# Performance work log

Measured on AMD Instinct MI355X. Metric: run time of the kernel, lower is better.

## Reference

```python
import jax, jax.numpy as jnp
import numpy as np
from jax import lax

CI, CO, K = 4096, 256, 4
COKK = CO * K * K  # 4096


def setup_inputs() -> dict:
    key = jax.random.key(0)
    k1, k2 = jax.random.split(key)
    U = jax.random.normal(k1, (CI, CI), dtype=jnp.float32) * 0.05
    V = jax.random.normal(k2, (COKK, COKK), dtype=jnp.float32) * 0.05
    return {"U": U, "V": V}


def _q(V):
    """Product of d Householder reflections H(v_0) ... H(v_{d-1}).
    Faithful to: M = I; for i in range(d): M = M @ (I - 2 v_i v_i^T),
    but applied as a rank-1 update M -= 2 (M v) v^T via lax.scan.
    """
    d = V.shape[0]
    # torch.norm(V.T, 2, dim=1) == column norms of V
    norms = jnp.linalg.norm(V, axis=0)
    Vn = V / norms[None, :]

    def step(M, v):
        Mv = M @ v  # [d]
        return M - 2.0 * jnp.outer(Mv, v), None

    M0 = jnp.eye(d, dtype=V.dtype)
    M, _ = lax.scan(step, M0, Vn.T)  # iterate over columns in order
    return M


def reference(U, V):
    Qu = _q(U)  # [ci, ci]
    Qv = _q(V)  # [cokk, cokk]
    if CI < COKK:
        W = Qu @ Qv[:CI, :]
    else:
        W = Qu[:, :COKK] @ Qv
    W = W.reshape(1, CI, CO, K, K)
    # original forward runs entirely under torch.no_grad()
    return lax.stop_gradient(W)
```

## Files before the change

kernel.cpp:

```cpp
#include <hip/hip_runtime.h>
#include <hip/hip_bf16.h>


#define N4K 4096
#define ELN ((long)N4K * (long)N4K)

typedef __bf16 bf16x8 __attribute__((ext_vector_type(8)));
typedef float f32x4 __attribute__((ext_vector_type(4)));

__device__ __forceinline__ unsigned short f2bf(float x) {
    unsigned int u = __builtin_bit_cast(unsigned int, x);
    u += 0x7FFFu + ((u >> 16) & 1u);
    return (unsigned short)(u >> 16);
}
__device__ __forceinline__ float bf2f(unsigned short h) {
    unsigned int u = ((unsigned int)h) << 16;
    return __builtin_bit_cast(float, u);
}
__device__ __forceinline__ void split_store(float v, unsigned short* H, unsigned short* L, long idx) {
    unsigned short h = f2bf(v);
    H[idx] = h;
    L[idx] = f2bf(v - bf2f(h));
}

__global__ __launch_bounds__(256) void colnorm2_k(const float* __restrict__ A, float* __restrict__ out) {
    int col = blockIdx.x * 256 + threadIdx.x;
    long r0 = (long)blockIdx.y * 128;
    float s = 0.f;
    for (int r = 0; r < 128; ++r) {
        float v = A[(r0 + r) * N4K + col];
        s += v * v;
    }
    atomicAdd(&out[col], s);
}

__global__ __launch_bounds__(256) void rsqrt_k(float* x) {
    int i = blockIdx.x * 256 + threadIdx.x;
    x[i] = 1.0f / sqrtf(x[i]);
}

__global__ __launch_bounds__(256) void normalize_split_k(const float* __restrict__ A, const float* __restrict__ rn,
                                                         unsigned short* __restrict__ H, unsigned short* __restrict__ L) {
    long i = ((long)blockIdx.x * 256 + threadIdx.x) * 4;
    float4 v = *(const float4*)(A + i);
    float4 rv = *(const float4*)(rn + (int)(i & (N4K - 1)));
    float a0 = v.x * rv.x, a1 = v.y * rv.y, a2 = v.z * rv.z, a3 = v.w * rv.w;
    ushort4 h, lo;
    h.x = f2bf(a0); lo.x = f2bf(a0 - bf2f(h.x));
    h.y = f2bf(a1); lo.y = f2bf(a1 - bf2f(h.y));
    h.z = f2bf(a2); lo.z = f2bf(a2 - bf2f(h.z));
    h.w = f2bf(a3); lo.w = f2bf(a3 - bf2f(h.w));
    *(ushort4*)(H + i) = h;
    *(ushort4*)(L + i) = lo;
}

__global__ __launch_bounds__(256) void transpose_split_k(const float* __restrict__ A, const float* __restrict__ rn,
                                                         unsigned short* __restrict__ H, unsigned short* __restrict__ L) {
    __shared__ float tile[64][65];
    int bj = blockIdx.x, bi = blockIdx.y;
    int t = threadIdx.x;
    int c = t & 63, r0 = t >> 6;
    for (int q = 0; q < 16; ++q) {
        int r = q * 4 + r0;
        tile[r][c] = A[(long)(bi * 64 + r) * N4K + bj * 64 + c];
    }
    __syncthreads();
    for (int q = 0; q < 16; ++q) {
        int orow = q * 4 + r0;
        int j = bj * 64 + orow;
        float v = tile[c][orow] * rn[j];
        long idx = (long)j * N4K + bi * 64 + c;
        unsigned short h = f2bf(v);
        H[idx] = h;
        L[idx] = f2bf(v - bf2f(h));
    }
}

__global__ __launch_bounds__(64) void tri_inv_base64_k(const unsigned short* __restrict__ Sh, const unsigned short* __restrict__ Sl,
                                                       unsigned short* __restrict__ Th, unsigned short* __restrict__ Tl,
                                                       unsigned short* __restrict__ Tth, unsigned short* __restrict__ Ttl) {
    __shared__ float R[64][65];
    __shared__ float X[64][65];
    int b0 = blockIdx.x * 64;
    int t = threadIdx.x;
    for (int r = 0; r < 64; ++r) {
        long idx = (long)(b0 + r) * N4K + b0 + t;
        float v = bf2f(Sh[idx]) + bf2f(Sl[idx]);
        R[r][t] = (t > r) ? v : 0.f;
    }
    __syncthreads();
    X[t][t] = 2.f;
    for (int i = t - 1; i >= 0; --i) {
        float s = 0.f;
        for (int k = i + 1; k <= t; ++k) s += R[i][k] * X[t][k];
        X[t][i] = -2.f * s;
    }
    __syncthreads();
    for (int r = 0; r < 64; ++r) {
        long idx = (long)(b0 + r) * N4K + b0 + t;
        float v = (t >= r) ? X[t][r] : 0.f;
        split_store(v, Th, Tl, idx);
        float vt = (r >= t) ? X[r][t] : 0.f;
        split_store(vt, Tth, Ttl, idx);
    }
}

__global__ __launch_bounds__(256) void combine64_k(const unsigned short* __restrict__ Sh, const unsigned short* __restrict__ Sl,
                                                   unsigned short* __restrict__ Th, unsigned short* __restrict__ Tl,
                                                   unsigned short* __restrict__ Tth, unsigned short* __restrict__ Ttl) {
    __shared__ float T11[64][65], T22[64][65], P[64][65];
    int p = blockIdx.x;
    int base = 128 * p;
    int t = threadIdx.x;
    for (int q = 0; q < 16; ++q) {
        int e = q * 256 + t;
        int r = e >> 6, c = e & 63;
        long i1 = (long)(base + r) * N4K + base + c;
        T11[r][c] = bf2f(Th[i1]) + bf2f(Tl[i1]);
        long i2 = (long)(base + 64 + r) * N4K + base + 64 + c;
        T22[r][c] = bf2f(Th[i2]) + bf2f(Tl[i2]);
    }
    __syncthreads();
    int j = t & 63, i0 = t >> 6;
    for (int i = i0; i < 64; i += 4) {
        float s = 0.f;
        for (int k = 0; k < 64; ++k) {
            long is = (long)(base + i) * N4K + base + 64 + k;
            float s12 = bf2f(Sh[is]) + bf2f(Sl[is]);
            s += s12 * T22[k][j];
        }
        P[i][j] = s;
    }
    __syncthreads();
    for (int i = i0; i < 64; i += 4) {
        float s = 0.f;
        for (int k = 0; k < 64; ++k) s += T11[i][k] * P[k][j];
        float v = -s;
        long it = (long)(base + i) * N4K + base + 64 + j;
        split_store(v, Th, Tl, it);
        long itt = (long)(base + 64 + j) * N4K + base + i;
        split_store(v, Tth, Ttl, itt);
    }
}

__global__ __launch_bounds__(256) void gemm_split_bt(
    const unsigned short* __restrict__ Ah, const unsigned short* __restrict__ Al, long lda, long sA,
    const unsigned short* __restrict__ Bh, const unsigned short* __restrict__ Bl, long ldb, long sB,
    float* __restrict__ Cf, unsigned short* __restrict__ Ch, unsigned short* __restrict__ Cl, long ldc, long sC,
    int K, float alpha, int addI) {
    __shared__ unsigned short sAh[128 * 32], sAl[128 * 32], sBh[128 * 32], sBl[128 * 32];
    int tid = threadIdx.x;
    int bx = blockIdx.x, by = blockIdx.y, bz = blockIdx.z;
    const unsigned short* pAh = Ah + (long)bz * sA + (long)by * 128 * lda;
    const unsigned short* pAl = Al + (long)bz * sA + (long)by * 128 * lda;
    const unsigned short* pBh = Bh + (long)bz * sB + (long)bx * 128 * ldb;
    const unsigned short* pBl = Bl + (long)bz * sB + (long)bx * 128 * ldb;
    int ilda = (int)lda, ildb = (int)ldb;

    int ch0 = tid, ch1 = tid + 256;
    int r0 = ch0 >> 2, c0 = ch0 & 3;
    int r1 = ch1 >> 2, c1 = ch1 & 3;
    int gA0 = r0 * ilda + c0 * 8, gA1 = r1 * ilda + c1 * 8;
    int gB0 = r0 * ildb + c0 * 8, gB1 = r1 * ildb + c1 * 8;
    int l0 = r0 * 32 + ((c0 ^ ((r0 >> 1) & 3)) << 3);
    int l1 = r1 * 32 + ((c1 ^ ((r1 >> 1) & 3)) << 3);

    int w = tid >> 6, l = tid & 63;
    int wm = w >> 1, wn = w & 1;
    int aoff[4], boff[4];
#pragma unroll
    for (int m = 0; m < 4; ++m) {
        int rowa = wm * 64 + m * 16 + (l & 15);
        aoff[m] = rowa * 32 + (((l >> 4) ^ ((rowa >> 1) & 3)) << 3);
        int rowb = wn * 64 + m * 16 + (l & 15);
        boff[m] = rowb * 32 + (((l >> 4) ^ ((rowb >> 1) & 3)) << 3);
    }

    f32x4 acc[4][4];
#pragma unroll
    for (int m = 0; m < 4; ++m)
#pragma unroll
        for (int n = 0; n < 4; ++n) acc[m][n] = (f32x4){0.f, 0.f, 0.f, 0.f};

    uint4 ra0 = *(const uint4*)(pAh + gA0), ra1 = *(const uint4*)(pAh + gA1);
    uint4 rb0 = *(const uint4*)(pAl + gA0), rb1 = *(const uint4*)(pAl + gA1);
    uint4 rc0 = *(const uint4*)(pBh + gB0), rc1 = *(const uint4*)(pBh + gB1);
    uint4 rd0 = *(const uint4*)(pBl + gB0), rd1 = *(const uint4*)(pBl + gB1);

    int nk = K >> 5;
#pragma unroll 1
    for (int kt = 0; kt < nk; ++kt) {
        __syncthreads();
        *(uint4*)&sAh[l0] = ra0; *(uint4*)&sAh[l1] = ra1;
        *(uint4*)&sAl[l0] = rb0; *(uint4*)&sAl[l1] = rb1;
        *(uint4*)&sBh[l0] = rc0; *(uint4*)&sBh[l1] = rc1;
        *(uint4*)&sBl[l0] = rd0; *(uint4*)&sBl[l1] = rd1;
        __syncthreads();
        if (kt + 1 < nk) {
            pAh += 32; pAl += 32; pBh += 32; pBl += 32;
            ra0 = *(const uint4*)(pAh + gA0); ra1 = *(const uint4*)(pAh + gA1);
            rb0 = *(const uint4*)(pAl + gA0); rb1 = *(const uint4*)(pAl + gA1);
            rc0 = *(const uint4*)(pBh + gB0); rc1 = *(const uint4*)(pBh + gB1);
            rd0 = *(const uint4*)(pBl + gB0); rd1 = *(const uint4*)(pBl + gB1);
        }
        bf16x8 fah[4], fal[4], fbh[4], fbl[4];
#pragma unroll
        for (int m = 0; m < 4; ++m) {
            fah[m] = *(const bf16x8*)&sAh[aoff[m]];
            fal[m] = *(const bf16x8*)&sAl[aoff[m]];
            fbh[m] = *(const bf16x8*)&sBh[boff[m]];
            fbl[m] = *(const bf16x8*)&sBl[boff[m]];
        }
#pragma unroll
        for (int m = 0; m < 4; ++m)
#pragma unroll
            for (int n = 0; n < 4; ++n) {
                acc[m][n] = __builtin_amdgcn_mfma_f32_16x16x32_bf16(fah[m], fbh[n], acc[m][n], 0, 0, 0);
                acc[m][n] = __builtin_amdgcn_mfma_f32_16x16x32_bf16(fah[m], fbl[n], acc[m][n], 0, 0, 0);
                acc[m][n] = __builtin_amdgcn_mfma_f32_16x16x32_bf16(fal[m], fbh[n], acc[m][n], 0, 0, 0);
            }
    }

    float* CfZ = Cf ? (Cf + (long)bz * sC) : nullptr;
    unsigned short* ChZ = Ch ? (Ch + (long)bz * sC) : nullptr;
    unsigned short* ClZ = Cl ? (Cl + (long)bz * sC) : nullptr;
    int r16 = (l >> 4) * 4, c16 = l & 15;
#pragma unroll
    for (int m = 0; m < 4; ++m)
#pragma unroll
        for (int n = 0; n < 4; ++n)
#pragma unroll
            for (int r = 0; r < 4; ++r) {
                int row = by * 128 + wm * 64 + m * 16 + r16 + r;
                int col = bx * 128 + wn * 64 + n * 16 + c16;
                float v = acc[m][n][r] * alpha;
                if (addI && row == col) v += 1.0f;
                long idx = (long)row * ldc + col;
                if (CfZ) CfZ[idx] = v;
                if (ChZ) {
                    unsigned short h = f2bf(v);
                    ChZ[idx] = h;
                    ClZ[idx] = f2bf(v - bf2f(h));
                }
            }
}

struct Bufs {
    unsigned short *Ah, *Al, *Th, *Tl, *Quh, *Qul, *Gh, *Gl;
    unsigned short *Sh, *Sl;
    float* rnorm;
};

static inline void launch_gemm(const unsigned short* Ah, const unsigned short* Al, long lda, long sA,
                               const unsigned short* Bh, const unsigned short* Bl, long ldb, long sB,
                               float* Cf, unsigned short* Ch, unsigned short* Cl, long ldc, long sC,
                               int M, int Nn, int K, float alpha, int addI, int Z, hipStream_t stream) {
    dim3 grid(Nn / 128, M / 128, Z);
    gemm_split_bt<<<grid, dim3(256), 0, stream>>>(Ah, Al, lda, sA, Bh, Bl, ldb, sB, Cf, Ch, Cl, ldc, sC, K, alpha, addI);
}

static void run_phase(const float* inp, const Bufs& B, bool left, hipStream_t s) {
    const size_t sz = (size_t)ELN * 2;
    unsigned short* Tth = B.Ah;
    unsigned short* Ttl = B.Al;
    hipMemsetAsync(B.rnorm, 0, N4K * sizeof(float), s);
    colnorm2_k<<<dim3(16, 32), dim3(256), 0, s>>>(inp, B.rnorm);
    rsqrt_k<<<dim3(16), dim3(256), 0, s>>>(B.rnorm);
    transpose_split_k<<<dim3(64, 64), dim3(256), 0, s>>>(inp, B.rnorm, B.Ah, B.Al);
    launch_gemm(B.Ah, B.Al, N4K, 0, B.Ah, B.Al, N4K, 0, nullptr, B.Sh, B.Sl, N4K, 0,
                N4K, N4K, N4K, 1.f, 0, 1, s);
    hipMemsetAsync(B.Th, 0, sz, s);
    hipMemsetAsync(B.Tl, 0, sz, s);
    hipMemsetAsync(Tth, 0, sz, s);
    hipMemsetAsync(Ttl, 0, sz, s);
    tri_inv_base64_k<<<dim3(64), dim3(64), 0, s>>>(B.Sh, B.Sl, B.Th, B.Tl, Tth, Ttl);
    combine64_k<<<dim3(32), dim3(256), 0, s>>>(B.Sh, B.Sl, B.Th, B.Tl, Tth, Ttl);
    for (int m = 128; m <= 2048; m <<= 1) {
        int Z = N4K / (2 * m);
        long sdiag = (long)2 * m * (N4K + 1);
        long offT22 = (long)m * (N4K + 1);
        launch_gemm(B.Th, B.Tl, N4K, sdiag, B.Sh + (long)m * N4K, B.Sl + (long)m * N4K, N4K, sdiag,
                    nullptr, B.Gh, B.Gl, m, (long)m * m, m, m, m, 1.f, 0, Z, s);
        launch_gemm(B.Gh, B.Gl, m, (long)m * m, Tth + offT22, Ttl + offT22, N4K, sdiag,
                    nullptr, B.Th + m, B.Tl + m, N4K, sdiag, m, m, m, -1.f, 0, Z, s);
        launch_gemm(Tth + offT22, Ttl + offT22, N4K, sdiag, B.Gh, B.Gl, m, (long)m * m,
                    nullptr, Tth + (long)m * N4K, Ttl + (long)m * N4K, N4K, sdiag, m, m, m, -1.f, 0, Z, s);
    }
    normalize_split_k<<<dim3(16384), dim3(256), 0, s>>>(inp, B.rnorm, B.Ah, B.Al);
    launch_gemm(B.Ah, B.Al, N4K, 0, B.Th, B.Tl, N4K, 0, nullptr, B.Sh, B.Sl, N4K, 0,
                N4K, N4K, N4K, 1.f, 0, 1, s);
    if (left) {
        launch_gemm(B.Ah, B.Al, N4K, 0, B.Sh, B.Sl, N4K, 0, nullptr, B.Quh, B.Qul, N4K, 0,
                    N4K, N4K, N4K, -1.f, 1, 1, s);
    } else {
        launch_gemm(B.Sh, B.Sl, N4K, 0, B.Ah, B.Al, N4K, 0, nullptr, B.Th, B.Tl, N4K, 0,
                    N4K, N4K, N4K, -1.f, 1, 1, s);
    }
}

extern "C" void kernel_launch(void* const* d_in, const int* in_sizes, int n_in,
                              void* d_out, int out_size, void* d_ws, size_t ws_size,
                              hipStream_t stream) {
    const float* U = (const float*)d_in[0];
    const float* V = (const float*)d_in[1];
    const size_t sz = (size_t)ELN * 2;
    const size_t gsz = (size_t)2048 * 2048 * 2;
    const size_t need = 6 * sz + 2 * gsz + (size_t)N4K * sizeof(float);
    if (ws_size < need) {
        hipMemsetAsync(d_out, 0, (size_t)out_size * sizeof(float), stream);
        return;
    }
    char* w = (char*)d_ws;
    Bufs B;
    B.Ah = (unsigned short*)w; w += sz;
    B.Al = (unsigned short*)w; w += sz;
    B.Th = (unsigned short*)w; w += sz;
    B.Tl = (unsigned short*)w; w += sz;
    B.Quh = (unsigned short*)w; w += sz;
    B.Qul = (unsigned short*)w; w += sz;
    B.Gh = (unsigned short*)w; w += gsz;
    B.Gl = (unsigned short*)w; w += gsz;
    B.rnorm = (float*)w; w += (size_t)N4K * sizeof(float);
    B.Sh = (unsigned short*)d_out;
    B.Sl = B.Sh + ELN;

    run_phase(U, B, true, stream);
    run_phase(V, B, false, stream);
    launch_gemm(B.Quh, B.Qul, N4K, 0, B.Th, B.Tl, N4K, 0, (float*)d_out, nullptr, nullptr, N4K, 0,
                N4K, N4K, N4K, 1.f, 0, 1, stream);
}
```

Baseline: 4.179 ms.

## Exploit symmetry and triangularity to skip zero K-tiles in split GEMMs

Adds per-block K-range bounds to the split-bf16 GEMM so that products involving triangular T factors iterate only over the nonzero K tiles. The Gram matrix GEMM now computes only the upper block triangle and mirrors each off-diagonal tile into the lower half with transposed vector stores. This removes roughly half of the MFMA and load work in the Gram, T-recursion and A·T GEMMs. The cost is load imbalance across blocks, idle early-exit blocks, and extra strided stores for the mirrored tiles.

```diff
diff --git a/kernel.cpp b/kernel.cpp
--- a/kernel.cpp
+++ b/kernel.cpp
@@ -147,14 +147,22 @@
     const unsigned short* __restrict__ Ah, const unsigned short* __restrict__ Al, long lda, long sA,
     const unsigned short* __restrict__ Bh, const unsigned short* __restrict__ Bl, long ldb, long sB,
     float* __restrict__ Cf, unsigned short* __restrict__ Ch, unsigned short* __restrict__ Cl, long ldc, long sC,
-    int K, float alpha, int addI) {
+    int K, float alpha, int addI,
+    int kt0m_by, int kt0m_bx, int ktem_by, int ktem_bx, int symm) {
     __shared__ unsigned short sAh[128 * 32], sAl[128 * 32], sBh[128 * 32], sBl[128 * 32];
     int tid = threadIdx.x;
     int bx = blockIdx.x, by = blockIdx.y, bz = blockIdx.z;
-    const unsigned short* pAh = Ah + (long)bz * sA + (long)by * 128 * lda;
-    const unsigned short* pAl = Al + (long)bz * sA + (long)by * 128 * lda;
-    const unsigned short* pBh = Bh + (long)bz * sB + (long)bx * 128 * ldb;
-    const unsigned short* pBl = Bl + (long)bz * sB + (long)bx * 128 * ldb;
+    if (symm && bx < by) return;
+    int nk = K >> 5;
+    int kt0 = kt0m_by * by + kt0m_bx * bx;
+    int kte = nk;
+    if (ktem_by) { int e = ktem_by * (by + 1); kte = e < kte ? e : kte; }
+    if (ktem_bx) { int e = ktem_bx * (bx + 1); kte = e < kte ? e : kte; }
+
+    const unsigned short* pAh = Ah + (long)bz * sA + (long)by * 128 * lda + (long)kt0 * 32;
+    const unsigned short* pAl = Al + (long)bz * sA + (long)by * 128 * lda + (long)kt0 * 32;
+    const unsigned short* pBh = Bh + (long)bz * sB + (long)bx * 128 * ldb + (long)kt0 * 32;
+    const unsigned short* pBl = Bl + (long)bz * sB + (long)bx * 128 * ldb + (long)kt0 * 32;
     int ilda = (int)lda, ildb = (int)ldb;
 
     int ch0 = tid, ch1 = tid + 256;
@@ -187,16 +195,15 @@
     uint4 rc0 = *(const uint4*)(pBh + gB0), rc1 = *(const uint4*)(pBh + gB1);
     uint4 rd0 = *(const uint4*)(pBl + gB0), rd1 = *(const uint4*)(pBl + gB1);
 
-    int nk = K >> 5;
 #pragma unroll 1
-    for (int kt = 0; kt < nk; ++kt) {
+    for (int kt = kt0; kt < kte; ++kt) {
         __syncthreads();
         *(uint4*)&sAh[l0] = ra0; *(uint4*)&sAh[l1] = ra1;
         *(uint4*)&sAl[l0] = rb0; *(uint4*)&sAl[l1] = rb1;
         *(uint4*)&sBh[l0] = rc0; *(uint4*)&sBh[l1] = rc1;
         *(uint4*)&sBl[l0] = rd0; *(uint4*)&sBl[l1] = rd1;
         __syncthreads();
-        if (kt + 1 < nk) {
+        if (kt + 1 < kte) {
             pAh += 32; pAl += 32; pBh += 32; pBl += 32;
             ra0 = *(const uint4*)(pAh + gA0); ra1 = *(const uint4*)(pAh + gA1);
             rb0 = *(const uint4*)(pAl + gA0); rb1 = *(const uint4*)(pAl + gA1);
@@ -243,6 +250,25 @@
                     ClZ[idx] = f2bf(v - bf2f(h));
                 }
             }
+    if (symm && bx > by && ChZ) {
+#pragma unroll
+        for (int m = 0; m < 4; ++m)
+#pragma unroll
+            for (int n = 0; n < 4; ++n) {
+                int mrow = bx * 128 + wn * 64 + n * 16 + c16;
+                int mcol = by * 128 + wm * 64 + m * 16 + r16;
+                ushort4 th, tl;
+                float v0 = acc[m][n][0] * alpha, v1 = acc[m][n][1] * alpha;
+                float v2 = acc[m][n][2] * alpha, v3 = acc[m][n][3] * alpha;
+                th.x = f2bf(v0); tl.x = f2bf(v0 - bf2f(th.x));
+                th.y = f2bf(v1); tl.y = f2bf(v1 - bf2f(th.y));
+                th.z = f2bf(v2); tl.z = f2bf(v2 - bf2f(th.z));
+                th.w = f2bf(v3); tl.w = f2bf(v3 - bf2f(th.w));
+                long midx = (long)mrow * ldc + mcol;
+                *(ushort4*)&ChZ[midx] = th;
+                *(ushort4*)&ClZ[midx] = tl;
+            }
+    }
 }
 
 struct Bufs {
@@ -254,9 +280,11 @@
 static inline void launch_gemm(const unsigned short* Ah, const unsigned short* Al, long lda, long sA,
                                const unsigned short* Bh, const unsigned short* Bl, long ldb, long sB,
                                float* Cf, unsigned short* Ch, unsigned short* Cl, long ldc, long sC,
-                               int M, int Nn, int K, float alpha, int addI, int Z, hipStream_t stream) {
+                               int M, int Nn, int K, float alpha, int addI, int Z, hipStream_t stream,
+                               int kt0m_by = 0, int kt0m_bx = 0, int ktem_by = 0, int ktem_bx = 0, int symm = 0) {
     dim3 grid(Nn / 128, M / 128, Z);
-    gemm_split_bt<<<grid, dim3(256), 0, stream>>>(Ah, Al, lda, sA, Bh, Bl, ldb, sB, Cf, Ch, Cl, ldc, sC, K, alpha, addI);
+    gemm_split_bt<<<grid, dim3(256), 0, stream>>>(Ah, Al, lda, sA, Bh, Bl, ldb, sB, Cf, Ch, Cl, ldc, sC,
+                                                  K, alpha, addI, kt0m_by, kt0m_bx, ktem_by, ktem_bx, symm);
 }
 
 static void run_phase(const float* inp, const Bufs& B, bool left, hipStream_t s) {
@@ -268,7 +296,7 @@
     rsqrt_k<<<dim3(16), dim3(256), 0, s>>>(B.rnorm);
     transpose_split_k<<<dim3(64, 64), dim3(256), 0, s>>>(inp, B.rnorm, B.Ah, B.Al);
     launch_gemm(B.Ah, B.Al, N4K, 0, B.Ah, B.Al, N4K, 0, nullptr, B.Sh, B.Sl, N4K, 0,
-                N4K, N4K, N4K, 1.f, 0, 1, s);
+                N4K, N4K, N4K, 1.f, 0, 1, s, 0, 0, 0, 0, 1);
     hipMemsetAsync(B.Th, 0, sz, s);
     hipMemsetAsync(B.Tl, 0, sz, s);
     hipMemsetAsync(Tth, 0, sz, s);
@@ -280,15 +308,15 @@
         long sdiag = (long)2 * m * (N4K + 1);
         long offT22 = (long)m * (N4K + 1);
         launch_gemm(B.Th, B.Tl, N4K, sdiag, B.Sh + (long)m * N4K, B.Sl + (long)m * N4K, N4K, sdiag,
-                    nullptr, B.Gh, B.Gl, m, (long)m * m, m, m, m, 1.f, 0, Z, s);
+                    nullptr, B.Gh, B.Gl, m, (long)m * m, m, m, m, 1.f, 0, Z, s, 4, 0, 0, 0, 0);
         launch_gemm(B.Gh, B.Gl, m, (long)m * m, Tth + offT22, Ttl + offT22, N4K, sdiag,
-                    nullptr, B.Th + m, B.Tl + m, N4K, sdiag, m, m, m, -1.f, 0, Z, s);
+                    nullptr, B.Th + m, B.Tl + m, N4K, sdiag, m, m, m, -1.f, 0, Z, s, 0, 0, 0, 4, 0);
         launch_gemm(Tth + offT22, Ttl + offT22, N4K, sdiag, B.Gh, B.Gl, m, (long)m * m,
-                    nullptr, Tth + (long)m * N4K, Ttl + (long)m * N4K, N4K, sdiag, m, m, m, -1.f, 0, Z, s);
+                    nullptr, Tth + (long)m * N4K, Ttl + (long)m * N4K, N4K, sdiag, m, m, m, -1.f, 0, Z, s, 0, 0, 4, 0, 0);
     }
     normalize_split_k<<<dim3(16384), dim3(256), 0, s>>>(inp, B.rnorm, B.Ah, B.Al);
     launch_gemm(B.Ah, B.Al, N4K, 0, B.Th, B.Tl, N4K, 0, nullptr, B.Sh, B.Sl, N4K, 0,
-                N4K, N4K, N4K, 1.f, 0, 1, s);
+                N4K, N4K, N4K, 1.f, 0, 1, s, 0, 4, 0, 0, 0);
     if (left) {
         launch_gemm(B.Ah, B.Al, N4K, 0, B.Sh, B.Sl, N4K, 0, nullptr, B.Quh, B.Qul, N4K, 0,
                     N4K, N4K, N4K, -1.f, 1, 1, s);
```

Result: faster. 3.914 ms (-6.3%).
